# Optimization experiments

Hardware: AMD Instinct MI355X
Metric: run time of the kernel (lower is better)

Reference implementation:

```python
import jax, jax.numpy as jnp
import numpy as np

D_MODEL = 1024
NUM_HEADS = 16
D_K = D_MODEL // NUM_HEADS


def setup_inputs() -> dict:
    key = jax.random.key(0)
    ks = jax.random.split(key, 11)
    B, S = 4, 2048
    s = 1.0 / np.sqrt(D_MODEL)
    inp = {
        'q': jax.random.normal(ks[0], (B, S, D_MODEL), dtype=jnp.float32),
        'k': jax.random.normal(ks[1], (B, S, D_MODEL), dtype=jnp.float32),
        'v': jax.random.normal(ks[2], (B, S, D_MODEL), dtype=jnp.float32),
        'Wq': jax.random.normal(ks[3], (D_MODEL, D_MODEL), dtype=jnp.float32) * s,
        'bq': jnp.zeros((D_MODEL,), dtype=jnp.float32),
        'Wk': jax.random.normal(ks[4], (D_MODEL, D_MODEL), dtype=jnp.float32) * s,
        'bk': jnp.zeros((D_MODEL,), dtype=jnp.float32),
        'Wv': jax.random.normal(ks[5], (D_MODEL, D_MODEL), dtype=jnp.float32) * s,
        'bv': jnp.zeros((D_MODEL,), dtype=jnp.float32),
        'Wo': jax.random.normal(ks[6], (D_MODEL, D_MODEL), dtype=jnp.float32) * s,
        'bo': jnp.zeros((D_MODEL,), dtype=jnp.float32),
    }
    return inp


def _split_heads(x):
    B, S, _ = x.shape
    return x.reshape(B, S, NUM_HEADS, D_K).transpose(0, 2, 1, 3)  # [B,H,S,d_k]


def reference(q, k, v, Wq, bq, Wk, bk, Wv, bv, Wo, bo):
    B, S, _ = q.shape
    qh = _split_heads(q @ Wq.T + bq)
    kh = _split_heads(k @ Wk.T + bk)
    vh = _split_heads(v @ Wv.T + bv)
    scale = 1.0 / jnp.sqrt(jnp.asarray(D_K, dtype=qh.dtype))
    scores = jnp.einsum('bhqd,bhkd->bhqk', qh, kh) * scale  # [B,H,S,S]
    attn = jax.nn.softmax(scores, axis=-1)
    out = jnp.einsum('bhqk,bhkd->bhqd', attn, vh)  # [B,H,S,d_k]
    out = out.transpose(0, 2, 1, 3).reshape(B, S, D_MODEL)
    return out @ Wo.T + bo
```

## Files before the change

kernel.cpp:

```cpp
#include <hip/hip_runtime.h>


typedef __bf16 bf16_t;
typedef bf16_t bf16x8 __attribute__((ext_vector_type(8)));
typedef bf16_t bf16x4 __attribute__((ext_vector_type(4)));
typedef float  f32x4  __attribute__((ext_vector_type(4)));
typedef short  s16x4  __attribute__((ext_vector_type(4)));

#define MFMA16(A, B, C) __builtin_amdgcn_mfma_f32_16x16x32_bf16(A, B, C, 0, 0, 0)

static __device__ __forceinline__ f32x4 mfma16k16(bf16x4 a, bf16x4 b, f32x4 c) {
  return __builtin_amdgcn_mfma_f32_16x16x16bf16_1k(
      __builtin_bit_cast(s16x4, a), __builtin_bit_cast(s16x4, b), c, 0, 0, 0);
}

#define NB   4
#define SEQ  2048
#define DM   1024
#define NH   16
#define DK   64
#define MTOT (NB * SEQ)
#define QSCALE 0.18033688011112042f

__device__ __forceinline__ void async_copy16(bf16_t* lds, const bf16_t* gsrc) {
  __builtin_amdgcn_global_load_lds(
      (const __attribute__((address_space(1))) unsigned int*)gsrc,
      (__attribute__((address_space(3))) unsigned int*)lds, 16, 0, 0);
}

__device__ __forceinline__ float fast_exp2(float x) {
#if __has_builtin(__builtin_amdgcn_exp2f)
  return __builtin_amdgcn_exp2f(x);
#else
  return exp2f(x);
#endif
}

__global__ __launch_bounds__(256) void cvt3(const float* __restrict__ a,
                                            const float* __restrict__ b,
                                            const float* __restrict__ c,
                                            bf16_t* __restrict__ oa,
                                            bf16_t* __restrict__ ob,
                                            bf16_t* __restrict__ oc, int n4) {
  const int z = blockIdx.y;
  const float* s = (z == 0) ? a : (z == 1) ? b : c;
  bf16_t* d = (z == 0) ? oa : (z == 1) ? ob : oc;
  int i = blockIdx.x * 256 + threadIdx.x;
  if (i < n4) {
    f32x4 v = ((const f32x4*)s)[i];
    ((bf16x4*)d)[i] = __builtin_convertvector(v, bf16x4);
  }
}

__global__ __launch_bounds__(256) void cvt4(const float* __restrict__ a,
                                            const float* __restrict__ b,
                                            const float* __restrict__ c,
                                            const float* __restrict__ dd,
                                            bf16_t* __restrict__ oa,
                                            bf16_t* __restrict__ ob,
                                            bf16_t* __restrict__ oc,
                                            bf16_t* __restrict__ od, int n4) {
  const int z = blockIdx.y;
  const float* s = (z == 0) ? a : (z == 1) ? b : (z == 2) ? c : dd;
  bf16_t* d = (z == 0) ? oa : (z == 1) ? ob : (z == 2) ? oc : od;
  int i = blockIdx.x * 256 + threadIdx.x;
  if (i < n4) {
    f32x4 v = ((const f32x4*)s)[i];
    ((bf16x4*)d)[i] = __builtin_convertvector(v, bf16x4);
  }
}

__device__ __forceinline__ void gemm_core_1024(const bf16_t* __restrict__ A,
                                               const bf16_t* __restrict__ W,
                                               bf16_t* sA, bf16_t* sB,
                                               f32x4 (&acc)[4][4], int m0, int n0) {
  const int tid = threadIdx.x;
  const int lane = tid & 63, r = lane & 15, qd = lane >> 4;
  const int wave = tid >> 6;
  const int wm = (wave & 1) * 64, wn = (wave >> 1) * 64;
  const int arow = tid >> 2, achk = (tid & 3) * 8;
  const bf16_t* gA = A + (size_t)(m0 + arow) * DM + achk;
  const bf16_t* gB = W + (size_t)(n0 + arow) * DM + achk;
  bf16_t* lA = sA + arow * 32 + achk;
  bf16_t* lB = sB + arow * 32 + achk;

  for (int k0 = 0; k0 < DM; k0 += 32) {
    __syncthreads();
    async_copy16(lA,           gA + k0);
    async_copy16(lA + 64 * 32, gA + k0 + (size_t)64 * DM);
    async_copy16(lB,           gB + k0);
    async_copy16(lB + 64 * 32, gB + k0 + (size_t)64 * DM);
    __syncthreads();

    bf16x8 af[4], bw[4];
#pragma unroll
    for (int i = 0; i < 4; i++)
      af[i] = *(const bf16x8*)(sA + (wm + i * 16 + r) * 32 + qd * 8);
#pragma unroll
    for (int j = 0; j < 4; j++)
      bw[j] = *(const bf16x8*)(sB + (wn + j * 16 + r) * 32 + qd * 8);
#pragma unroll
    for (int i = 0; i < 4; i++)
#pragma unroll
      for (int j = 0; j < 4; j++)
        acc[i][j] = MFMA16(af[i], bw[j], acc[i][j]);
  }
}

__global__ __launch_bounds__(256)
void gemm_qkv(const bf16_t* __restrict__ qb, const bf16_t* __restrict__ kb,
              const bf16_t* __restrict__ vb, const bf16_t* __restrict__ wq,
              const bf16_t* __restrict__ wk, const bf16_t* __restrict__ wv,
              const float* __restrict__ bq, const float* __restrict__ bk,
              const float* __restrict__ bv, bf16_t* __restrict__ Qh,
              bf16_t* __restrict__ Kh, bf16_t* __restrict__ Vt) {
  __shared__ __align__(16) bf16_t sA[128 * 32];
  __shared__ __align__(16) bf16_t sB[128 * 32];
  const int z = blockIdx.z;
  const bf16_t* A = (z == 0) ? qb : (z == 1) ? kb : vb;
  const bf16_t* W = (z == 0) ? wq : (z == 1) ? wk : wv;
  const float* bias = (z == 0) ? bq : (z == 1) ? bk : bv;
  const int m0 = blockIdx.y * 128, n0 = blockIdx.x * 128;

  f32x4 acc[4][4] = {};
  gemm_core_1024(A, W, sA, sB, acc, m0, n0);

  const int tid = threadIdx.x, lane = tid & 63, r = lane & 15, qd = lane >> 4;
  const int wave = tid >> 6, wm = (wave & 1) * 64, wn = (wave >> 1) * 64;
#pragma unroll
  for (int j = 0; j < 4; j++) {
    const int n = n0 + wn + j * 16 + r;
    const float bs = bias[n];
    const int h = n >> 6, d = n & 63;
#pragma unroll
    for (int i = 0; i < 4; i++) {
#pragma unroll
      for (int rr = 0; rr < 4; rr++) {
        const int m = m0 + wm + i * 16 + qd * 4 + rr;
        const int b_ = m >> 11, s_ = m & 2047;
        float v = acc[i][j][rr] + bs;
        if (z == 0) {
          v *= QSCALE;
          Qh[(((size_t)b_ * NH + h) * SEQ + s_) * DK + d] = (bf16_t)v;
        } else if (z == 1) {
          Kh[(((size_t)b_ * NH + h) * SEQ + s_) * DK + d] = (bf16_t)v;
        } else {
          Vt[(((size_t)b_ * NH + h) * DK + d) * SEQ + s_] = (bf16_t)v;
        }
      }
    }
  }
}

__global__ __launch_bounds__(256)
void gemm_out(const bf16_t* __restrict__ A, const bf16_t* __restrict__ W,
              const float* __restrict__ bias, float* __restrict__ C) {
  __shared__ __align__(16) bf16_t sA[128 * 32];
  __shared__ __align__(16) bf16_t sB[128 * 32];
  const int m0 = blockIdx.y * 128, n0 = blockIdx.x * 128;
  f32x4 acc[4][4] = {};
  gemm_core_1024(A, W, sA, sB, acc, m0, n0);

  const int tid = threadIdx.x, lane = tid & 63, r = lane & 15, qd = lane >> 4;
  const int wave = tid >> 6, wm = (wave & 1) * 64, wn = (wave >> 1) * 64;
#pragma unroll
  for (int j = 0; j < 4; j++) {
    const int n = n0 + wn + j * 16 + r;
    const float bs = bias[n];
#pragma unroll
    for (int i = 0; i < 4; i++) {
#pragma unroll
      for (int rr = 0; rr < 4; rr++) {
        const int m = m0 + wm + i * 16 + qd * 4 + rr;
        C[(size_t)m * DM + n] = acc[i][j][rr] + bs;
      }
    }
  }
}

__global__ __launch_bounds__(256)
void attn(const bf16_t* __restrict__ Qh, const bf16_t* __restrict__ Kh,
          const bf16_t* __restrict__ Vt, bf16_t* __restrict__ Ah) {
  __shared__ __align__(16) bf16_t sK[2][128 * 64];
  __shared__ __align__(16) bf16_t sV[2][64 * 128];

  const int tid = threadIdx.x, wave = tid >> 6, lane = tid & 63;
  const int r = lane & 15, qd = lane >> 4;
  const int bh = blockIdx.y;
  const int q0 = blockIdx.x * 128 + wave * 32;
  const size_t bK = (size_t)bh * SEQ * DK;
  const size_t bV = (size_t)bh * DK * SEQ;

  bf16x8 aq[2][2];
#pragma unroll
  for (int qt = 0; qt < 2; qt++)
#pragma unroll
    for (int hf = 0; hf < 2; hf++)
      aq[qt][hf] = *(const bf16x8*)(Qh + bK + (size_t)(q0 + qt * 16 + r) * DK +
                                    hf * 32 + qd * 8);

  f32x4 o[4][2] = {};
  float lsum[2] = {0.f, 0.f};

  const int krow = tid >> 3, kc = tid & 7;
  const int vrow = tid >> 4, vc = tid & 15;

  const bf16_t* gK = Kh + bK + (size_t)krow * DK + ((kc ^ (krow & 7)) * 8);
  const bf16_t* gV = Vt + bV + (size_t)vrow * SEQ + ((vc ^ (vrow & 15)) * 8);

#define STAGE(buf, kv0)                                                        \
  do {                                                                         \
    _Pragma("unroll") for (int it_ = 0; it_ < 4; it_++)                        \
        async_copy16(&sK[buf][0] + it_ * 2048 + tid * 8,                       \
                     gK + (size_t)(kv0 + it_ * 32) * DK);                      \
    _Pragma("unroll") for (int it_ = 0; it_ < 4; it_++)                        \
        async_copy16(&sV[buf][0] + it_ * 2048 + tid * 8,                       \
                     gV + (size_t)it_ * 16 * SEQ + (kv0));                     \
  } while (0)

  STAGE(0, 0);

  for (int it = 0; it < 16; it++) {
    const int buf = it & 1;
    __syncthreads();
    if (it < 15) STAGE(buf ^ 1, (it + 1) * 128);

    const bf16_t* K0 = &sK[buf][0];
    const bf16_t* V0 = &sV[buf][0];

    f32x4 s[2][8];
#pragma unroll
    for (int mt = 0; mt < 8; mt++) {
      const int row = mt * 16 + r;
      bf16x8 ka0 = *(const bf16x8*)(K0 + row * 64 + ((qd ^ (r & 7)) * 8));
      bf16x8 ka1 = *(const bf16x8*)(K0 + row * 64 + (((4 + qd) ^ (r & 7)) * 8));
#pragma unroll
      for (int qt = 0; qt < 2; qt++) {
        f32x4 t = {0.f, 0.f, 0.f, 0.f};
        t = MFMA16(ka0, aq[qt][0], t);
        t = MFMA16(ka1, aq[qt][1], t);
        s[qt][mt] = t;
      }
    }

    bf16x4 p[2][8];
#pragma unroll
    for (int qt = 0; qt < 2; qt++) {
      float ls = 0.f;
#pragma unroll
      for (int mt = 0; mt < 8; mt++) {
        f32x4 e;
#pragma unroll
        for (int rr = 0; rr < 4; rr++) {
          e[rr] = fast_exp2(s[qt][mt][rr]);
          ls += e[rr];
        }
        p[qt][mt] = __builtin_convertvector(e, bf16x4);
      }
      lsum[qt] += ls;
    }

#pragma unroll
    for (int dt = 0; dt < 4; dt++) {
      const int d = dt * 16 + r;
#pragma unroll
      for (int mt = 0; mt < 8; mt++) {
        const int cc = (mt * 2 + (qd >> 1)) ^ r;
        bf16x4 va = *(const bf16x4*)(V0 + d * 128 + cc * 8 + (qd & 1) * 4);
#pragma unroll
        for (int qt = 0; qt < 2; qt++)
          o[dt][qt] = mfma16k16(va, p[qt][mt], o[dt][qt]);
      }
    }
  }

  float linv[2];
#pragma unroll
  for (int qt = 0; qt < 2; qt++) {
    float l = lsum[qt];
    l += __shfl_xor(l, 16);
    l += __shfl_xor(l, 32);
    linv[qt] = 1.0f / l;
  }
  const int b_ = bh >> 4, h_ = bh & 15;
#pragma unroll
  for (int qt = 0; qt < 2; qt++) {
    const size_t rowbase = ((size_t)b_ * SEQ + q0 + qt * 16 + r) * DM + h_ * DK;
#pragma unroll
    for (int dt = 0; dt < 4; dt++) {
      f32x4 w = o[dt][qt] * linv[qt];
      *(bf16x4*)(Ah + rowbase + dt * 16 + qd * 4) =
          __builtin_convertvector(w, bf16x4);
    }
  }
}

extern "C" void kernel_launch(void* const* d_in, const int* in_sizes, int n_in,
                              void* d_out, int out_size, void* d_ws,
                              size_t ws_size, hipStream_t stream) {
  const float* q  = (const float*)d_in[0];
  const float* k  = (const float*)d_in[1];
  const float* v  = (const float*)d_in[2];
  const float* Wq = (const float*)d_in[3];
  const float* bq = (const float*)d_in[4];
  const float* Wk = (const float*)d_in[5];
  const float* bk = (const float*)d_in[6];
  const float* Wv = (const float*)d_in[7];
  const float* bv = (const float*)d_in[8];
  const float* Wo = (const float*)d_in[9];
  const float* bo = (const float*)d_in[10];

  char* ws = (char*)d_ws;
  const size_t SZ_QKV = (size_t)MTOT * DM * 2;
  const size_t SZ_W   = (size_t)DM * DM * 2;
  bf16_t* qb  = (bf16_t*)(ws);
  bf16_t* kb_ = (bf16_t*)(ws + SZ_QKV);
  bf16_t* vb  = (bf16_t*)(ws + 2 * SZ_QKV);
  bf16_t* Wqb = (bf16_t*)(ws + 3 * SZ_QKV);
  bf16_t* Wkb = (bf16_t*)(ws + 3 * SZ_QKV + SZ_W);
  bf16_t* Wvb = (bf16_t*)(ws + 3 * SZ_QKV + 2 * SZ_W);
  bf16_t* Wob = (bf16_t*)(ws + 3 * SZ_QKV + 3 * SZ_W);
  bf16_t* Qh  = (bf16_t*)(ws + 3 * SZ_QKV + 4 * SZ_W);
  bf16_t* Kh  = (bf16_t*)(ws + 4 * SZ_QKV + 4 * SZ_W);
  bf16_t* Vt  = (bf16_t*)(ws + 5 * SZ_QKV + 4 * SZ_W);
  bf16_t* Ah  = (bf16_t*)(ws + 6 * SZ_QKV + 4 * SZ_W);

  const int n4_qkv = MTOT * DM / 4;
  const int n4_w   = DM * DM / 4;
  cvt3<<<dim3(n4_qkv / 256, 3), 256, 0, stream>>>(q, k, v, qb, kb_, vb, n4_qkv);
  cvt4<<<dim3(n4_w / 256, 4), 256, 0, stream>>>(Wq, Wk, Wv, Wo, Wqb, Wkb, Wvb,
                                                Wob, n4_w);

  gemm_qkv<<<dim3(8, 64, 3), 256, 0, stream>>>(qb, kb_, vb, Wqb, Wkb, Wvb, bq,
                                               bk, bv, Qh, Kh, Vt);

  attn<<<dim3(16, 64), 256, 0, stream>>>(Qh, Kh, Vt, Ah);

  gemm_out<<<dim3(8, 64), 256, 0, stream>>>(Ah, Wob, bo, (float*)d_out);
}
```

Measured before the change: 388.2 us.

## Double-buffer LDS tiles in projection GEMMs and swap block raster order

The shared GEMM core now keeps two LDS stages. It prefetches the next K-slice with async copies while the MFMAs run on the current one, and drops the second barrier per iteration. This is meant to hide global-load latency behind compute, at the cost of doubling LDS per block, which could lower occupancy. The QKV and output GEMM grids are also transposed so that consecutive blocks walk along M for a fixed N tile, which changes the cache reuse pattern.

```diff
diff --git a/kernel.cpp b/kernel.cpp
--- a/kernel.cpp
+++ b/kernel.cpp
@@ -84,27 +84,37 @@
   bf16_t* lA = sA + arow * 32 + achk;
   bf16_t* lB = sB + arow * 32 + achk;
 
+#define GSTAGE(buf, k0)                                                       \
+  do {                                                                        \
+    async_copy16(lA + (buf) * 4096,           gA + (k0));                     \
+    async_copy16(lA + (buf) * 4096 + 64 * 32, gA + (k0) + (size_t)64 * DM);   \
+    async_copy16(lB + (buf) * 4096,           gB + (k0));                     \
+    async_copy16(lB + (buf) * 4096 + 64 * 32, gB + (k0) + (size_t)64 * DM);   \
+  } while (0)
+
+  GSTAGE(0, 0);
+#pragma unroll 2
   for (int k0 = 0; k0 < DM; k0 += 32) {
+    const int buf = (k0 >> 5) & 1;
     __syncthreads();
-    async_copy16(lA,           gA + k0);
-    async_copy16(lA + 64 * 32, gA + k0 + (size_t)64 * DM);
-    async_copy16(lB,           gB + k0);
-    async_copy16(lB + 64 * 32, gB + k0 + (size_t)64 * DM);
-    __syncthreads();
-
+    if (k0 + 32 < DM) GSTAGE(buf ^ 1, k0 + 32);
+
+    const bf16_t* cA = sA + buf * 4096;
+    const bf16_t* cB = sB + buf * 4096;
     bf16x8 af[4], bw[4];
 #pragma unroll
     for (int i = 0; i < 4; i++)
-      af[i] = *(const bf16x8*)(sA + (wm + i * 16 + r) * 32 + qd * 8);
+      af[i] = *(const bf16x8*)(cA + (wm + i * 16 + r) * 32 + qd * 8);
 #pragma unroll
     for (int j = 0; j < 4; j++)
-      bw[j] = *(const bf16x8*)(sB + (wn + j * 16 + r) * 32 + qd * 8);
+      bw[j] = *(const bf16x8*)(cB + (wn + j * 16 + r) * 32 + qd * 8);
 #pragma unroll
     for (int i = 0; i < 4; i++)
 #pragma unroll
       for (int j = 0; j < 4; j++)
         acc[i][j] = MFMA16(af[i], bw[j], acc[i][j]);
   }
+#undef GSTAGE
 }
 
 __global__ __launch_bounds__(256)
@@ -114,13 +124,13 @@
               const float* __restrict__ bq, const float* __restrict__ bk,
               const float* __restrict__ bv, bf16_t* __restrict__ Qh,
               bf16_t* __restrict__ Kh, bf16_t* __restrict__ Vt) {
-  __shared__ __align__(16) bf16_t sA[128 * 32];
-  __shared__ __align__(16) bf16_t sB[128 * 32];
+  __shared__ __align__(16) bf16_t sA[2 * 128 * 32];
+  __shared__ __align__(16) bf16_t sB[2 * 128 * 32];
   const int z = blockIdx.z;
   const bf16_t* A = (z == 0) ? qb : (z == 1) ? kb : vb;
   const bf16_t* W = (z == 0) ? wq : (z == 1) ? wk : wv;
   const float* bias = (z == 0) ? bq : (z == 1) ? bk : bv;
-  const int m0 = blockIdx.y * 128, n0 = blockIdx.x * 128;
+  const int m0 = blockIdx.x * 128, n0 = blockIdx.y * 128;
 
   f32x4 acc[4][4] = {};
   gemm_core_1024(A, W, sA, sB, acc, m0, n0);
@@ -155,9 +165,9 @@
 __global__ __launch_bounds__(256)
 void gemm_out(const bf16_t* __restrict__ A, const bf16_t* __restrict__ W,
               const float* __restrict__ bias, float* __restrict__ C) {
-  __shared__ __align__(16) bf16_t sA[128 * 32];
-  __shared__ __align__(16) bf16_t sB[128 * 32];
-  const int m0 = blockIdx.y * 128, n0 = blockIdx.x * 128;
+  __shared__ __align__(16) bf16_t sA[2 * 128 * 32];
+  __shared__ __align__(16) bf16_t sB[2 * 128 * 32];
+  const int m0 = blockIdx.x * 128, n0 = blockIdx.y * 128;
   f32x4 acc[4][4] = {};
   gemm_core_1024(A, W, sA, sB, acc, m0, n0);
 
@@ -331,10 +341,10 @@
   cvt4<<<dim3(n4_w / 256, 4), 256, 0, stream>>>(Wq, Wk, Wv, Wo, Wqb, Wkb, Wvb,
                                                 Wob, n4_w);
 
-  gemm_qkv<<<dim3(8, 64, 3), 256, 0, stream>>>(qb, kb_, vb, Wqb, Wkb, Wvb, bq,
+  gemm_qkv<<<dim3(64, 8, 3), 256, 0, stream>>>(qb, kb_, vb, Wqb, Wkb, Wvb, bq,
                                                bk, bv, Qh, Kh, Vt);
 
   attn<<<dim3(16, 64), 256, 0, stream>>>(Qh, Kh, Vt, Ah);
 
-  gemm_out<<<dim3(8, 64), 256, 0, stream>>>(Ah, Wob, bo, (float*)d_out);
-}
+  gemm_out<<<dim3(64, 8), 256, 0, stream>>>(Ah, Wob, bo, (float*)d_out);
+}
```

Result: faster. 379.2 us (-2.3%).
